# Kernel optimization log

Hardware: AMD Instinct MI355X
Metric: run time of the kernel (lower is better)

The kernel has to match this reference:

```python
import jax, jax.numpy as jnp
import numpy as np

S_LEN = 1024; HIDDEN = 2048; VOCAB = 32000; DFF = 6144
NK = 8; NV = 16; DK = 128; DV = 128; CONV_K = 4
CONV_DIM = 2 * NK * DK + NV * DV  # 4096
NQ = 16; NKV = 2; HD = 128; MAX_KV = 4096; SP = 512; CHUNK = 64


def silu(x):
    return x * jax.nn.sigmoid(x)


def rmsnorm(x, w, eps=1e-6):
    xf = x.astype(jnp.float32)
    return (xf * jax.lax.rsqrt(jnp.mean(xf * xf, -1, keepdims=True) + eps)) * w


def gated_rmsnorm(x, z, w, eps=1e-6):
    xf = x.astype(jnp.float32) * silu(z.astype(jnp.float32))
    return (xf * jax.lax.rsqrt(jnp.mean(xf * xf, -1, keepdims=True) + eps)) * w


def rotate_half(x):
    a, b = jnp.split(x, 2, -1)
    return jnp.concatenate([-b, a], -1)


def chunk_gated_delta_rule(q, k, v, g, beta, init_state, chunk=CHUNK):
    # q,k: [B,S,H,Dk]; v: [B,S,H,Dv]; g,beta: [B,S,H]; init_state: [B,H,Dk,Dv]
    q = q / jnp.sqrt(jnp.sum(q * q, -1, keepdims=True) + 1e-6)  # qk l2norm
    k = k / jnp.sqrt(jnp.sum(k * k, -1, keepdims=True) + 1e-6)
    tr = lambda x: x.transpose(0, 2, 1, 3).astype(jnp.float32)
    q, k, v = tr(q), tr(k), tr(v)
    g = g.transpose(0, 2, 1).astype(jnp.float32)
    beta = beta.transpose(0, 2, 1).astype(jnp.float32)
    B, H, S, Dk = q.shape
    Dv = v.shape[-1]
    N = S // chunk  # S is a multiple of chunk here (no padding needed)
    q = q * Dk ** -0.5
    rc = lambda x: x.reshape(B, H, N, chunk, x.shape[-1])
    q, k, v = rc(q), rc(k), rc(v)
    g = jnp.cumsum(g.reshape(B, H, N, chunk), -1)  # cumulative log-decay within chunk
    beta = beta.reshape(B, H, N, chunk)
    kb = k * beta[..., None]
    vb = v * beta[..., None]
    ii = jnp.arange(chunk)
    lower = ii[:, None] >= ii[None, :]
    strict = ii[:, None] > ii[None, :]
    decay = jnp.where(lower, jnp.exp(g[..., :, None] - g[..., None, :]), 0.0)
    # strictly-lower A; T = (I - A)^{-1} (exact triangular solve == converged Neumann series)
    A = -jnp.where(strict, jnp.einsum('bhnik,bhnjk->bhnij', kb, k) * decay, 0.0)
    eye = jnp.eye(chunk, dtype=jnp.float32)
    T = jax.scipy.linalg.solve_triangular(eye - A, jnp.broadcast_to(eye, A.shape), lower=True)
    w = jnp.einsum('bhnij,bhnjd->bhnid', T, vb)
    kc = jnp.einsum('bhnij,bhnjd->bhnid', T, kb * jnp.exp(g)[..., None])
    mv = lambda x: jnp.moveaxis(x, 2, 0)

    def step(state, xs):
        qi, ki, wi, kci, gi, di = xs
        attn = jnp.where(lower, jnp.einsum('bhik,bhjk->bhij', qi, ki) * di, 0.0)
        v_new = wi - jnp.einsum('bhik,bhkd->bhid', kci, state)
        out = jnp.einsum('bhik,bhkd->bhid', qi * jnp.exp(gi)[..., None], state) \
            + jnp.einsum('bhij,bhjd->bhid', attn, v_new)
        gl = gi[..., -1]
        kd = ki * jnp.exp(gl[..., None] - gi)[..., None]
        state = state * jnp.exp(gl)[..., None, None] + jnp.einsum('bhik,bhid->bhkd', kd, v_new)
        return state, out

    final, outs = jax.lax.scan(step, init_state.astype(jnp.float32),
                               (mv(q), mv(k), mv(w), mv(kc), mv(g), mv(decay)))
    out = jnp.moveaxis(outs, 0, 2).reshape(B, H, S, Dv).transpose(0, 2, 1, 3)  # [B,S,H,Dv]
    return out, final


def mlp(x, gw, uw, dw):
    return (silu(x @ gw) * (x @ uw)) @ dw


def model_forward(input_ids, start_pos, rope_cos, rope_sin, attn_mask, conv_state, rec_state,
                  key_cache, value_cache, embed_w, dl_ln_w, dl_qkv_w, conv_w, conv_b, dl_z_w,
                  dl_b_w, dl_a_w, A_log, dt_bias, dn_norm_w, dl_out_w, dl_post_ln_w, dl_gate_w,
                  dl_up_w, dl_down_w, al_ln_w, q_w, q_norm_w, k_w, k_norm_w, v_w, o_w,
                  al_post_ln_w, al_gate_w, al_up_w, al_down_w, final_norm_w, lm_head_w):
    B, S = input_ids.shape
    hidden = embed_w[input_ids]
    # ---------------- DeltaNet (linear attention) layer ----------------
    res = hidden
    x = rmsnorm(hidden, dl_ln_w)
    mixed = (x @ dl_qkv_w).transpose(0, 2, 1)             # [B, CONV_DIM, S]
    padded = jnp.concatenate([conv_state, mixed], -1)      # [B, CONV_DIM, K+S]
    L = padded.shape[-1] - (CONV_K - 1)
    conv = conv_b[:, None] + sum(conv_w[:, kk][:, None] * padded[:, :, kk:kk + L]
                                 for kk in range(CONV_K))  # depthwise conv1d
    mixed = silu(conv[:, :, -S:]).transpose(0, 2, 1)
    new_conv = padded[:, :, -CONV_K:]
    kd = NK * DK
    qq = mixed[..., :kd].reshape(B, S, NK, DK)
    kk_ = mixed[..., kd:2 * kd].reshape(B, S, NK, DK)
    vv = mixed[..., 2 * kd:].reshape(B, S, NV, DV)
    z = (x @ dl_z_w).reshape(B, S, NV, DV)
    beta = jax.nn.sigmoid(x @ dl_b_w)
    a = (x @ dl_a_w).astype(jnp.float32)
    g = -jnp.exp(A_log.astype(jnp.float32)) * jax.nn.softplus(a + dt_bias)
    rep = NV // NK
    qq = jnp.repeat(qq, rep, axis=2)
    kk_ = jnp.repeat(kk_, rep, axis=2)
    core, new_rec = chunk_gated_delta_rule(qq, kk_, vv, g, beta, rec_state)
    core = gated_rmsnorm(core.reshape(-1, DV), z.reshape(-1, DV), dn_norm_w).reshape(B, S, NV * DV)
    hidden = res + core @ dl_out_w
    hidden = hidden + mlp(rmsnorm(hidden, dl_post_ln_w), dl_gate_w, dl_up_w, dl_down_w)
    # ---------------- Full attention layer (gated GQA, KV-cache scatter) ----------------
    res = hidden
    x = rmsnorm(hidden, al_ln_w)
    qg = (x @ q_w).reshape(B, S, NQ, 2 * HD)
    query, gate = jnp.split(qg, 2, -1)
    gate = gate.reshape(B, S, NQ * HD)
    query = rmsnorm(query, q_norm_w).transpose(0, 2, 1, 3)               # [B,NQ,S,HD]
    key_new = rmsnorm((x @ k_w).reshape(B, S, NKV, HD), k_norm_w).transpose(0, 2, 1, 3)
    value_new = (x @ v_w).reshape(B, S, NKV, HD).transpose(0, 2, 1, 3)
    c = rope_cos[:, None]
    sn = rope_sin[:, None]
    query = query * c + rotate_half(query) * sn
    key_new = key_new * c + rotate_half(key_new) * sn
    new_kc = jax.lax.dynamic_update_slice(key_cache, key_new, (0, 0, start_pos, 0))
    new_vc = jax.lax.dynamic_update_slice(value_cache, value_new, (0, 0, start_pos, 0))
    ng = NQ // NKV
    k_rep = jnp.repeat(new_kc, ng, axis=1)
    v_rep = jnp.repeat(new_vc, ng, axis=1)
    scores = jnp.einsum('bhsd,bhtd->bhst', query, k_rep) * HD ** -0.5 + attn_mask
    probs = jax.nn.softmax(scores.astype(jnp.float32), -1).astype(query.dtype)
    ao = jnp.einsum('bhst,bhtd->bhsd', probs, v_rep).transpose(0, 2, 1, 3).reshape(B, S, NQ * HD)
    ao = ao * jax.nn.sigmoid(gate)
    hidden = res + ao @ o_w
    hidden = hidden + mlp(rmsnorm(hidden, al_post_ln_w), al_gate_w, al_up_w, al_down_w)
    logits = rmsnorm(hidden, final_norm_w) @ lm_head_w
    return logits, new_conv, new_rec, new_kc, new_vc


def setup_inputs():
    key = jax.random.key(0)
    ks = iter(jax.random.split(key, 64))
    def rn(shape, s=0.02):
        return jax.random.normal(next(ks), shape, jnp.float32) * s
    input_ids = jax.random.randint(next(ks), (1, S_LEN), 0, VOCAB)
    inv = 1.0 / (10000.0 ** (jnp.arange(0, HD, 2, dtype=jnp.float32) / HD))
    pos = jnp.arange(SP, SP + S_LEN, dtype=jnp.float32)
    fr = pos[:, None] * inv[None, :]
    emb = jnp.concatenate([fr, fr], -1)
    rope_cos = jnp.cos(emb)[None]
    rope_sin = jnp.sin(emb)[None]
    qpos = SP + jnp.arange(S_LEN)
    kpos = jnp.arange(MAX_KV)
    attn_mask = jnp.where(kpos[None, :] <= qpos[:, None], 0.0, -1e9).astype(jnp.float32)[None, None]
    return dict(
        input_ids=input_ids, seq_len=S_LEN, start_pos=SP,
        rope_cos=rope_cos, rope_sin=rope_sin, attn_mask=attn_mask,
        conv_state=rn((1, CONV_DIM, CONV_K), 1.0), rec_state=rn((1, NV, DK, DV), 1.0),
        key_cache=rn((1, NKV, MAX_KV, HD), 1.0), value_cache=rn((1, NKV, MAX_KV, HD), 1.0),
        embed_w=rn((VOCAB, HIDDEN)), dl_ln_w=jnp.ones(HIDDEN),
        dl_qkv_w=rn((HIDDEN, CONV_DIM)), conv_w=rn((CONV_DIM, CONV_K), 0.3),
        conv_b=rn((CONV_DIM,)), dl_z_w=rn((HIDDEN, NV * DV)),
        dl_b_w=rn((HIDDEN, NV)), dl_a_w=rn((HIDDEN, NV)),
        A_log=jnp.log(jnp.linspace(1.0, 8.0, NV)), dt_bias=rn((NV,), 0.1),
        dn_norm_w=jnp.ones(DV), dl_out_w=rn((NV * DV, HIDDEN)),
        dl_post_ln_w=jnp.ones(HIDDEN), dl_gate_w=rn((HIDDEN, DFF)),
        dl_up_w=rn((HIDDEN, DFF)), dl_down_w=rn((DFF, HIDDEN)),
        al_ln_w=jnp.ones(HIDDEN), q_w=rn((HIDDEN, NQ * HD * 2)), q_norm_w=jnp.ones(HD),
        k_w=rn((HIDDEN, NKV * HD)), k_norm_w=jnp.ones(HD), v_w=rn((HIDDEN, NKV * HD)),
        o_w=rn((NQ * HD, HIDDEN)), al_post_ln_w=jnp.ones(HIDDEN),
        al_gate_w=rn((HIDDEN, DFF)), al_up_w=rn((HIDDEN, DFF)), al_down_w=rn((DFF, HIDDEN)),
        final_norm_w=jnp.ones(HIDDEN), lm_head_w=rn((HIDDEN, VOCAB)))


def reference(input_ids, seq_len, start_pos, rope_cos, rope_sin, attn_mask, conv_state,
              rec_state, key_cache, value_cache, embed_w, dl_ln_w, dl_qkv_w, conv_w, conv_b,
              dl_z_w, dl_b_w, dl_a_w, A_log, dt_bias, dn_norm_w, dl_out_w, dl_post_ln_w,
              dl_gate_w, dl_up_w, dl_down_w, al_ln_w, q_w, q_norm_w, k_w, k_norm_w, v_w, o_w,
              al_post_ln_w, al_gate_w, al_up_w, al_down_w, final_norm_w, lm_head_w):
    del seq_len  # unused in original forward body (padding bookkeeping only)
    return model_forward(input_ids, start_pos, rope_cos, rope_sin, attn_mask, conv_state,
                         rec_state, key_cache, value_cache, embed_w, dl_ln_w, dl_qkv_w, conv_w,
                         conv_b, dl_z_w, dl_b_w, dl_a_w, A_log, dt_bias, dn_norm_w, dl_out_w,
                         dl_post_ln_w, dl_gate_w, dl_up_w, dl_down_w, al_ln_w, q_w, q_norm_w,
                         k_w, k_norm_w, v_w, o_w, al_post_ln_w, al_gate_w, al_up_w, al_down_w,
                         final_norm_w, lm_head_w)
```

## Files before the change

### kernel.cpp

```cpp
#include <hip/hip_runtime.h>
#include <math.h>

#define S_LEN 1024
#define HIDN  2048
#define NVH   16
#define CDIM  4096
#define MAXKV 4096
#define SP    512

typedef __attribute__((ext_vector_type(4))) float f32x4v;
typedef _Float16 f16x8 __attribute__((ext_vector_type(8)));
typedef unsigned short ushort_t;

__device__ __forceinline__ unsigned int pack2h(float a, float b) {
  auto h = __builtin_amdgcn_cvt_pkrtz(a, b);
  return __builtin_bit_cast(unsigned int, h);
}
__device__ __forceinline__ ushort_t h16(float x) {
  auto v = __builtin_amdgcn_cvt_pkrtz(x, x);
  return (ushort_t)__builtin_bit_cast(unsigned int, v);
}
__device__ __forceinline__ void gload16(const void* g, void* l) {
  __builtin_amdgcn_global_load_lds(
      (const __attribute__((address_space(1))) void*)(g),
      (__attribute__((address_space(3))) void*)(l), 16, 0, 0);
}

template<int TM, bool ACC>
__global__ __launch_bounds__(256) void gemm_h(const ushort_t* __restrict__ A16,
    const float* __restrict__ B, float* __restrict__ C, int M, int N, int K) {
  constexpr int MI = TM / 32;
  __shared__ ushort_t Al[TM * 32];
  __shared__ unsigned int Bl[4][128][4];
  const int tid = threadIdx.x;
  const int gm = M / TM;
  const int nwg = gridDim.x;
  const int q = nwg >> 3, r = nwg & 7;
  const int xcd = blockIdx.x & 7, ii = blockIdx.x >> 3;
  const int lin = (xcd < r) ? (xcd * (q + 1) + ii)
                            : (r * (q + 1) + (xcd - r) * q + ii);
  const int m0 = (lin % gm) * TM;
  const int n0 = (lin / gm) * 128;
  const int wave = tid >> 6, lane = tid & 63;
  const int wm = (wave >> 1) * (TM / 2), wn = (wave & 1) * 64;
  const int lr = lane & 15, lg = lane >> 4;
  const int bn = tid & 127, bkb = (tid >> 7) * 2;
  const size_t panstride = (size_t)(K >> 5) * 2048;
  const ushort_t* Apan = A16 + (size_t)(m0 >> 6) * panstride;
  const float* Bp = B + (size_t)(bkb * 8) * N + n0 + bn;
  float br[16];
  f32x4v acc[MI][4];
  #pragma unroll
  for (int i = 0; i < MI; ++i)
    #pragma unroll
    for (int j = 0; j < 4; ++j)
      #pragma unroll
      for (int r2 = 0; r2 < 4; ++r2) acc[i][j][r2] = 0.f;
  const int NT = K >> 5;
  #pragma unroll
  for (int j = 0; j < 16; ++j) br[j] = Bp[(size_t)j * N];
  for (int t = 0; t < NT; ++t) {
    __syncthreads();
    if (TM == 128) {
      #pragma unroll
      for (int i2 = 0; i2 < 2; ++i2) {
        int c = wave * 2 + i2;
        int kb = c >> 1, half = c & 1;
        gload16(Apan + half * panstride + (size_t)t * 2048 + kb * 512 + lane * 8,
                Al + kb * 1024 + half * 512);
      }
    } else {
      int kb = wave;
      gload16(Apan + (size_t)t * 2048 + kb * 512 + lane * 8, Al + kb * 512);
    }
    *(uint4*)&Bl[bkb][bn][0] = make_uint4(
        pack2h(br[0], br[1]), pack2h(br[2], br[3]),
        pack2h(br[4], br[5]), pack2h(br[6], br[7]));
    *(uint4*)&Bl[bkb + 1][bn][0] = make_uint4(
        pack2h(br[8], br[9]), pack2h(br[10], br[11]),
        pack2h(br[12], br[13]), pack2h(br[14], br[15]));
    if (t + 1 < NT) {
      Bp += (size_t)32 * N;
      #pragma unroll
      for (int j = 0; j < 16; ++j) br[j] = Bp[(size_t)j * N];
    }
    __syncthreads();
    f16x8 af[MI], bfr[4];
    #pragma unroll
    for (int mi = 0; mi < MI; ++mi)
      af[mi] = *(const f16x8*)&Al[lg * (TM * 8) + (wm + mi * 16 + lr) * 8];
    #pragma unroll
    for (int ni = 0; ni < 4; ++ni)
      bfr[ni] = *(const f16x8*)&Bl[lg][wn + ni * 16 + lr][0];
    #pragma unroll
    for (int mi = 0; mi < MI; ++mi)
      #pragma unroll
      for (int ni = 0; ni < 4; ++ni)
        acc[mi][ni] = __builtin_amdgcn_mfma_f32_16x16x32_f16(
            af[mi], bfr[ni], acc[mi][ni], 0, 0, 0);
  }
  #pragma unroll
  for (int mi = 0; mi < MI; ++mi) {
    #pragma unroll
    for (int ni = 0; ni < 4; ++ni) {
      const int rr = m0 + wm + mi * 16 + lg * 4;
      const int cc = n0 + wn + ni * 16 + lr;
      #pragma unroll
      for (int r2 = 0; r2 < 4; ++r2) {
        float* cp = C + (size_t)(rr + r2) * N + cc;
        if (ACC) *cp += acc[mi][ni][r2];
        else     *cp = acc[mi][ni][r2];
      }
    }
  }
}

template<int TM, bool ACC, bool FS>
__global__ __launch_bounds__(256) void gemm_f16(const float* __restrict__ A,
    const float* A2, const float* __restrict__ B,
    float* __restrict__ C, int M, int N, int K) {
  constexpr int MI = TM / 32;
  constexpr int AF = TM / 8;
  __shared__ unsigned int Al[4][TM][4];
  __shared__ unsigned int Bl[4][128][4];
  const int tid = threadIdx.x;
  const int gm = M / TM;
  const int nwg = gridDim.x;
  const int q = nwg >> 3, r = nwg & 7;
  const int xcd = blockIdx.x & 7, ii = blockIdx.x >> 3;
  const int lin = (xcd < r) ? (xcd * (q + 1) + ii)
                            : (r * (q + 1) + (xcd - r) * q + ii);
  const int m0 = (lin % gm) * TM;
  const int n0 = (lin / gm) * 128;
  const int wave = tid >> 6, lane = tid & 63;
  const int wm = (wave >> 1) * (TM / 2), wn = (wave & 1) * 64;
  const int lr = lane & 15, lg = lane >> 4;
  const int am  = (TM == 128) ? (tid >> 1) : (tid >> 2);
  const int akb = (TM == 128) ? ((tid & 1) * 2) : (tid & 3);
  const int bn = tid & 127, bkb = (tid >> 7) * 2;
  const float* Ap  = A + (size_t)(m0 + am) * K + akb * 8;
  const float* A2p = A2 + (size_t)(m0 + am) * K + akb * 8;
  const float* Bp = B + (size_t)(bkb * 8) * N + n0 + bn;
  float ar[AF], ar2[FS ? AF : 1], br[16];
  f32x4v acc[MI][4];
  #pragma unroll
  for (int i = 0; i < MI; ++i)
    #pragma unroll
    for (int j = 0; j < 4; ++j)
      #pragma unroll
      for (int r2 = 0; r2 < 4; ++r2) acc[i][j][r2] = 0.f;
  const int NT = K >> 5;
  #pragma unroll
  for (int q2 = 0; q2 < AF / 4; ++q2)
    *(float4*)&ar[q2 * 4] = *(const float4*)(Ap + q2 * 4);
  if (FS) {
    #pragma unroll
    for (int q2 = 0; q2 < AF / 4; ++q2)
      *(float4*)&ar2[q2 * 4] = *(const float4*)(A2p + q2 * 4);
  }
  #pragma unroll
  for (int j = 0; j < 16; ++j) br[j] = Bp[(size_t)j * N];
  for (int t = 0; t < NT; ++t) {
    __syncthreads();
    float av[AF];
    #pragma unroll
    for (int u = 0; u < AF; ++u) {
      float g = ar[u];
      av[u] = FS ? (g / (1.f + expf(-g))) * ar2[u] : g;
    }
    *(uint4*)&Al[akb][am][0] = make_uint4(
        pack2h(av[0], av[1]), pack2h(av[2], av[3]),
        pack2h(av[4], av[5]), pack2h(av[6], av[7]));
    if (TM == 128) {
      *(uint4*)&Al[akb + 1][am][0] = make_uint4(
          pack2h(av[8], av[9]), pack2h(av[10], av[11]),
          pack2h(av[12], av[13]), pack2h(av[14], av[15]));
    }
    *(uint4*)&Bl[bkb][bn][0] = make_uint4(
        pack2h(br[0], br[1]), pack2h(br[2], br[3]),
        pack2h(br[4], br[5]), pack2h(br[6], br[7]));
    *(uint4*)&Bl[bkb + 1][bn][0] = make_uint4(
        pack2h(br[8], br[9]), pack2h(br[10], br[11]),
        pack2h(br[12], br[13]), pack2h(br[14], br[15]));
    if (t + 1 < NT) {
      Ap += 32; A2p += 32; Bp += (size_t)32 * N;
      #pragma unroll
      for (int q2 = 0; q2 < AF / 4; ++q2)
        *(float4*)&ar[q2 * 4] = *(const float4*)(Ap + q2 * 4);
      if (FS) {
        #pragma unroll
        for (int q2 = 0; q2 < AF / 4; ++q2)
          *(float4*)&ar2[q2 * 4] = *(const float4*)(A2p + q2 * 4);
      }
      #pragma unroll
      for (int j = 0; j < 16; ++j) br[j] = Bp[(size_t)j * N];
    }
    __syncthreads();
    f16x8 af[MI], bfr[4];
    #pragma unroll
    for (int mi = 0; mi < MI; ++mi)
      af[mi] = *(const f16x8*)&Al[lg][wm + mi * 16 + lr][0];
    #pragma unroll
    for (int ni = 0; ni < 4; ++ni)
      bfr[ni] = *(const f16x8*)&Bl[lg][wn + ni * 16 + lr][0];
    #pragma unroll
    for (int mi = 0; mi < MI; ++mi)
      #pragma unroll
      for (int ni = 0; ni < 4; ++ni)
        acc[mi][ni] = __builtin_amdgcn_mfma_f32_16x16x32_f16(
            af[mi], bfr[ni], acc[mi][ni], 0, 0, 0);
  }
  #pragma unroll
  for (int mi = 0; mi < MI; ++mi) {
    #pragma unroll
    for (int ni = 0; ni < 4; ++ni) {
      const int rr = m0 + wm + mi * 16 + lg * 4;
      const int cc = n0 + wn + ni * 16 + lr;
      #pragma unroll
      for (int r2 = 0; r2 < 4; ++r2) {
        float* cp = C + (size_t)(rr + r2) * N + cc;
        if (ACC) *cp += acc[mi][ni][r2];
        else     *cp = acc[mi][ni][r2];
      }
    }
  }
}

__global__ __launch_bounds__(256) void embed_k(const int* __restrict__ ids,
    const float* __restrict__ emb, float* __restrict__ hid) {
  int t = blockIdx.x * 256 + threadIdx.x;
  int s = t >> 9;
  int c4 = (t & 511) * 4;
  *(float4*)(hid + (size_t)s * HIDN + c4) =
      *(const float4*)(emb + (size_t)ids[s] * HIDN + c4);
}

__global__ __launch_bounds__(256) void rmsnorm_k(const float* __restrict__ in,
    const float* __restrict__ w, float* __restrict__ out,
    ushort_t* __restrict__ x16) {
  const int row = blockIdx.x;
  const float* ip = in + (size_t)row * HIDN;
  float ss = 0.f;
  for (int c = threadIdx.x * 4; c < HIDN; c += 1024) {
    float4 v = *(const float4*)(ip + c);
    ss += v.x * v.x + v.y * v.y + v.z * v.z + v.w * v.w;
  }
  #pragma unroll
  for (int o = 32; o > 0; o >>= 1) ss += __shfl_down(ss, o, 64);
  __shared__ float sred[4];
  if ((threadIdx.x & 63) == 0) sred[threadIdx.x >> 6] = ss;
  __syncthreads();
  float tot = sred[0] + sred[1] + sred[2] + sred[3];
  float sc = 1.f / sqrtf(tot * (1.f / HIDN) + 1e-6f);
  const int m = row & 63, mp = row >> 6;
  ushort_t* xb = x16 + (size_t)mp * (HIDN >> 5) * 2048 + m * 8;
  for (int c = threadIdx.x * 4; c < HIDN; c += 1024) {
    float4 v = *(const float4*)(ip + c);
    float4 o = make_float4(v.x * sc * w[c], v.y * sc * w[c + 1],
                           v.z * sc * w[c + 2], v.w * sc * w[c + 3]);
    *(float4*)(out + (size_t)row * HIDN + c) = o;
    int kt = c >> 5, kb = (c >> 3) & 3, j = c & 7;
    *(uint2*)(xb + (size_t)kt * 2048 + kb * 512 + j) =
        make_uint2(pack2h(o.x, o.y), pack2h(o.z, o.w));
  }
}

__global__ __launch_bounds__(256) void newconv_k(const float* __restrict__ mixed,
                                                 float* __restrict__ nc) {
  int t = blockIdx.x * 256 + threadIdx.x;
  int c = t >> 2, kk = t & 3;
  nc[t] = mixed[(size_t)(1020 + kk) * CDIM + c];
}

__global__ __launch_bounds__(256) void conv_k(const float* __restrict__ mixed,
    const float* __restrict__ cstate, const float* __restrict__ cw,
    const float* __restrict__ cb, float* __restrict__ convo) {
  int idx = blockIdx.x * 256 + threadIdx.x;
  int c = idx & (CDIM - 1);
  int s = idx >> 12;
  float acc = cb[c];
  #pragma unroll
  for (int kk = 0; kk < 4; ++kk) {
    int j = s + 1 + kk;
    float pv = (j < 4) ? cstate[c * 4 + j] : mixed[(size_t)(j - 4) * CDIM + c];
    acc = fmaf(cw[c * 4 + kk], pv, acc);
  }
  convo[(size_t)s * CDIM + c] = acc / (1.f + expf(-acc));
}

__global__ __launch_bounds__(128) void qknorm_k(const float* __restrict__ convo,
    float* __restrict__ qn, float* __restrict__ kn) {
  const int b = blockIdx.x;
  const int h8 = b & 7, s = b >> 3;
  const int d = threadIdx.x;
  float qv = convo[(size_t)s * CDIM + h8 * 128 + d];
  float kv = convo[(size_t)s * CDIM + 1024 + h8 * 128 + d];
  __shared__ float sred[4];
  float pq = qv * qv, pk = kv * kv;
  #pragma unroll
  for (int o = 32; o > 0; o >>= 1) { pq += __shfl_down(pq, o, 64); pk += __shfl_down(pk, o, 64); }
  if ((d & 63) == 0) { sred[d >> 6] = pq; sred[2 + (d >> 6)] = pk; }
  __syncthreads();
  float sq = sred[0] + sred[1], sk = sred[2] + sred[3];
  qn[((size_t)h8 * S_LEN + s) * 128 + d] = qv * (1.f / sqrtf(sq + 1e-6f)) * 0.08838834764831845f;
  kn[((size_t)h8 * S_LEN + s) * 128 + d] = kv * (1.f / sqrtf(sk + 1e-6f));
}

__global__ __launch_bounds__(256) void betag_k(const float* __restrict__ x,
    const float* __restrict__ bw, const float* __restrict__ aw,
    const float* __restrict__ A_log, const float* __restrict__ dt_bias,
    float* __restrict__ beta, float* __restrict__ g) {
  __shared__ float sx[2048];
  __shared__ float rb[16][17], ra[16][17];
  const int s = blockIdx.x;
  for (int c = threadIdx.x; c < HIDN; c += 256) sx[c] = x[(size_t)s * HIDN + c];
  __syncthreads();
  const int h = threadIdx.x & 15, part = threadIdx.x >> 4;
  float accb = 0.f, acca = 0.f;
  for (int j = 0; j < 128; ++j) {
    int k = part * 128 + j;
    float xv = sx[k];
    accb = fmaf(xv, bw[(size_t)k * 16 + h], accb);
    acca = fmaf(xv, aw[(size_t)k * 16 + h], acca);
  }
  rb[part][h] = accb; ra[part][h] = acca;
  __syncthreads();
  if (threadIdx.x < 16) {
    const int hh = threadIdx.x;
    float sb = 0.f, sa = 0.f;
    for (int p = 0; p < 16; ++p) { sb += rb[p][hh]; sa += ra[p][hh]; }
    beta[(size_t)s * 16 + hh] = 1.f / (1.f + expf(-sb));
    float aa = sa + dt_bias[hh];
    float sp = (aa > 20.f) ? aa : log1pf(expf(aa));
    g[(size_t)s * 16 + hh] = -expf(A_log[hh]) * sp;
  }
}

__global__ __launch_bounds__(256) void delta_phase1(
    const float* __restrict__ qn, const float* __restrict__ kn,
    const float* __restrict__ convo, const float* __restrict__ beta,
    const float* __restrict__ g,
    float* __restrict__ Wb, ushort_t* __restrict__ KC16,
    ushort_t* __restrict__ Q16, ushort_t* __restrict__ K16,
    ushort_t* __restrict__ ATT16, float* __restrict__ GCb) {
  __shared__ float sK[64][129];
  __shared__ float sV[64][129];
  __shared__ float sQ[64][129];
  __shared__ float sT[64][64];
  __shared__ float sgc[64], sbeta[64], seg[64], sEgl[64];
  const int blk = blockIdx.x;
  const int n = blk & 15, h = blk >> 4;
  const int hq = h >> 1;
  const int r0 = n * 64;
  const int tid = threadIdx.x;
  const size_t hn = (size_t)h * 16 + n;
  for (int t = tid; t < 2048; t += 256) {
    int i = t >> 5, c4 = (t & 31) * 4;
    float4 kv = *(const float4*)(kn + ((size_t)hq * S_LEN + r0 + i) * 128 + c4);
    float4 qv = *(const float4*)(qn + ((size_t)hq * S_LEN + r0 + i) * 128 + c4);
    float4 vv = *(const float4*)(convo + (size_t)(r0 + i) * CDIM + 2048 + h * 128 + c4);
    sK[i][c4+0]=kv.x; sK[i][c4+1]=kv.y; sK[i][c4+2]=kv.z; sK[i][c4+3]=kv.w;
    sQ[i][c4+0]=qv.x; sQ[i][c4+1]=qv.y; sQ[i][c4+2]=qv.z; sQ[i][c4+3]=qv.w;
    sV[i][c4+0]=vv.x; sV[i][c4+1]=vv.y; sV[i][c4+2]=vv.z; sV[i][c4+3]=vv.w;
  }
  if (tid < 64) sbeta[tid] = beta[(size_t)(r0 + tid) * NVH + h];
  __syncthreads();
  if (tid == 0) {
    float acc = 0.f;
    for (int i = 0; i < 64; ++i) { acc += g[(size_t)(r0 + i) * NVH + h]; sgc[i] = acc; }
  }
  __syncthreads();
  if (tid < 64) {
    seg[tid] = expf(sgc[tid]);
    sEgl[tid] = expf(sgc[63] - sgc[tid]);
  }
  {
    const int ty = tid >> 4, tx = tid & 15;
    float a[4][4] = {};
    #pragma unroll 4
    for (int k = 0; k < 128; ++k) {
      float kr[4], kc_[4];
      #pragma unroll
      for (int di = 0; di < 4; ++di) kr[di] = sK[ty * 4 + di][k];
      #pragma unroll
      for (int dj = 0; dj < 4; ++dj) kc_[dj] = sK[tx * 4 + dj][k];
      #pragma unroll
      for (int di = 0; di < 4; ++di)
        #pragma unroll
        for (int dj = 0; dj < 4; ++dj)
          a[di][dj] = fmaf(kr[di], kc_[dj], a[di][dj]);
    }
    #pragma unroll
    for (int di = 0; di < 4; ++di) {
      int i = ty * 4 + di;
      #pragma unroll
      for (int dj = 0; dj < 4; ++dj) {
        int j = tx * 4 + dj;
        float v;
        if (i > j) v = sbeta[i] * a[di][dj] * expf(sgc[i] - sgc[j]);
        else v = (i == j) ? 1.f : 0.f;
        sT[i][j] = v;
      }
    }
  }
  __syncthreads();
  if (tid < 64) {
    const int c = tid;
    for (int i = 1; i < 64; ++i) {
      if (c <= i) {
        float acc = (c == i) ? 1.f : 0.f;
        for (int j = c; j < i; ++j) acc -= sT[i][j] * sT[j][c];
        sT[i][c] = acc;
      }
    }
  }
  __syncthreads();
  for (int t = tid; t < 1024; t += 256) {
    int i = t >> 4, dg = (t & 15) * 8;
    float aw[8] = {}, ak[8] = {};
    for (int j = 0; j <= i; ++j) {
      float tv = sT[i][j] * sbeta[j];
      float te = tv * seg[j];
      #pragma unroll
      for (int u = 0; u < 8; ++u) {
        aw[u] = fmaf(tv, sV[j][dg + u], aw[u]);
        ak[u] = fmaf(te, sK[j][dg + u], ak[u]);
      }
    }
    float* wp = Wb + (hn * 64 + i) * 128 + dg;
    *(float4*)wp = make_float4(aw[0], aw[1], aw[2], aw[3]);
    *(float4*)(wp + 4) = make_float4(aw[4], aw[5], aw[6], aw[7]);
    uint4 kc = make_uint4(pack2h(-ak[0], -ak[1]), pack2h(-ak[2], -ak[3]),
                          pack2h(-ak[4], -ak[5]), pack2h(-ak[6], -ak[7]));
    *(uint4*)(KC16 + hn * 8192 + (dg >> 3) * 512 + i * 8) = kc;
  }
  for (int t = tid; t < 1024; t += 256) {
    int i = t >> 4, dg = (t & 15) * 8;
    float e = seg[i];
    uint4 qv = make_uint4(
        pack2h(sQ[i][dg] * e, sQ[i][dg + 1] * e),
        pack2h(sQ[i][dg + 2] * e, sQ[i][dg + 3] * e),
        pack2h(sQ[i][dg + 4] * e, sQ[i][dg + 5] * e),
        pack2h(sQ[i][dg + 6] * e, sQ[i][dg + 7] * e));
    *(uint4*)(Q16 + hn * 8192 + (dg >> 3) * 512 + i * 8) = qv;
  }
  for (int t = tid; t < 1024; t += 256) {
    int kv = t & 127, ib = t >> 7;
    int i0 = ib * 8;
    uint4 kk2 = make_uint4(
        pack2h(sK[i0 + 0][kv] * sEgl[i0 + 0], sK[i0 + 1][kv] * sEgl[i0 + 1]),
        pack2h(sK[i0 + 2][kv] * sEgl[i0 + 2], sK[i0 + 3][kv] * sEgl[i0 + 3]),
        pack2h(sK[i0 + 4][kv] * sEgl[i0 + 4], sK[i0 + 5][kv] * sEgl[i0 + 5]),
        pack2h(sK[i0 + 6][kv] * sEgl[i0 + 6], sK[i0 + 7][kv] * sEgl[i0 + 7]));
    *(uint4*)(K16 + hn * 8192 + ib * 1024 + kv * 8) = kk2;
  }
  __syncthreads();
  {
    const int ty = tid >> 4, tx = tid & 15;
    float a[4][4] = {};
    #pragma unroll 4
    for (int k = 0; k < 128; ++k) {
      float qr[4], kc_[4];
      #pragma unroll
      for (int di = 0; di < 4; ++di) qr[di] = sQ[ty * 4 + di][k];
      #pragma unroll
      for (int dj = 0; dj < 4; ++dj) kc_[dj] = sK[tx * 4 + dj][k];
      #pragma unroll
      for (int di = 0; di < 4; ++di)
        #pragma unroll
        for (int dj = 0; dj < 4; ++dj)
          a[di][dj] = fmaf(qr[di], kc_[dj], a[di][dj]);
    }
    #pragma unroll
    for (int di = 0; di < 4; ++di) {
      int i = ty * 4 + di;
      #pragma unroll
      for (int dj = 0; dj < 4; ++dj) {
        int j = tx * 4 + dj;
        float v = 0.f;
        if (i >= j) v = a[di][dj] * expf(sgc[i] - sgc[j]);
        sT[i][j] = v;
      }
    }
  }
  __syncthreads();
  for (int t = tid; t < 512; t += 256) {
    int i = t >> 3, jb = t & 7;
    const float* ap = &sT[i][jb * 8];
    uint4 av = make_uint4(pack2h(ap[0], ap[1]), pack2h(ap[2], ap[3]),
                          pack2h(ap[4], ap[5]), pack2h(ap[6], ap[7]));
    *(uint4*)(ATT16 + hn * 4096 + jb * 512 + i * 8) = av;
  }
  if (tid < 64) GCb[hn * 64 + tid] = sgc[tid];
}

__global__ __launch_bounds__(256) void delta_phase2(
    const ushort_t* __restrict__ KC16, const ushort_t* __restrict__ Q16,
    const ushort_t* __restrict__ K16, const ushort_t* __restrict__ ATT16,
    const float* __restrict__ Wb, const float* __restrict__ GCb,
    const float* __restrict__ rec_state,
    float* __restrict__ core, float* __restrict__ new_rec) {
  __shared__ uint4 bufKC[1024];
  __shared__ uint4 bufQ[1024];
  __shared__ uint4 bufK[1024];
  __shared__ uint4 bufA[512];
  __shared__ uint4 bufS[512];
  __shared__ uint4 bufV[256];
  ushort_t* sKC = (ushort_t*)bufKC;
  ushort_t* sQ6 = (ushort_t*)bufQ;
  ushort_t* sK6 = (ushort_t*)bufK;
  ushort_t* sAT = (ushort_t*)bufA;
  ushort_t* sS  = (ushort_t*)bufS;
  ushort_t* sVn = (ushort_t*)bufV;
  const int h = blockIdx.x >> 2, ds = blockIdx.x & 3;
  const int d0 = ds * 32;
  const int tid = threadIdx.x;
  const int w = tid >> 6;
  const int lane = tid & 63, lr = lane & 15, lg = lane >> 4;
  const int rowS0 = w * 32;
  f32x4v aS[2][2];
  #pragma unroll
  for (int tm = 0; tm < 2; ++tm)
    #pragma unroll
    for (int tn = 0; tn < 2; ++tn)
      #pragma unroll
      for (int r = 0; r < 4; ++r) {
        int row = rowS0 + tm * 16 + lg * 4 + r;
        int col = tn * 16 + lr;
        aS[tm][tn][r] = rec_state[((size_t)h * 128 + row) * 128 + d0 + col];
      }
  for (int n = 0; n < 16; ++n) {
    const size_t hn = (size_t)h * 16 + n;
    const uint4* pKC = (const uint4*)(KC16 + hn * 8192);
    const uint4* pQ  = (const uint4*)(Q16  + hn * 8192);
    const uint4* pK  = (const uint4*)(K16  + hn * 8192);
    const uint4* pA  = (const uint4*)(ATT16 + hn * 4096);
    uint4 stKC[4], stQ[4], stK[4], stA[2];
    #pragma unroll
    for (int u = 0; u < 4; ++u) {
      stKC[u] = pKC[tid + u * 256];
      stQ[u]  = pQ[tid + u * 256];
      stK[u]  = pK[tid + u * 256];
    }
    #pragma unroll
    for (int u = 0; u < 2; ++u) stA[u] = pA[tid + u * 256];
    const float egl = expf(GCb[hn * 64 + 63]);
    float wseed[2][4];
    #pragma unroll
    for (int tn = 0; tn < 2; ++tn)
      #pragma unroll
      for (int r = 0; r < 4; ++r)
        wseed[tn][r] = Wb[(hn * 64 + (w * 16 + lg * 4 + r)) * 128 + d0 + tn * 16 + lr];
    #pragma unroll
    for (int tm = 0; tm < 2; ++tm)
      #pragma unroll
      for (int tn = 0; tn < 2; ++tn)
        #pragma unroll
        for (int r = 0; r < 4; ++r) {
          int row = rowS0 + tm * 16 + lg * 4 + r;
          int col = tn * 16 + lr;
          sS[(row >> 3) * 256 + col * 8 + (row & 7)] = h16(aS[tm][tn][r]);
        }
    #pragma unroll
    for (int u = 0; u < 4; ++u) {
      bufKC[tid + u * 256] = stKC[u];
      bufQ[tid + u * 256]  = stQ[u];
      bufK[tid + u * 256]  = stK[u];
    }
    #pragma unroll
    for (int u = 0; u < 2; ++u) bufA[tid + u * 256] = stA[u];
    __syncthreads();
    f32x4v aV[2];
    #pragma unroll
    for (int tn = 0; tn < 2; ++tn)
      #pragma unroll
      for (int r = 0; r < 4; ++r) aV[tn][r] = wseed[tn][r];
    #pragma unroll
    for (int c = 0; c < 4; ++c) {
      f16x8 a = *(const f16x8*)&sKC[((c * 4 + lg) * 64 + w * 16 + lr) * 8];
      #pragma unroll
      for (int tn = 0; tn < 2; ++tn) {
        f16x8 b = *(const f16x8*)&sS[((c * 4 + lg) * 32 + tn * 16 + lr) * 8];
        aV[tn] = __builtin_amdgcn_mfma_f32_16x16x32_f16(a, b, aV[tn], 0, 0, 0);
      }
    }
    #pragma unroll
    for (int tn = 0; tn < 2; ++tn)
      #pragma unroll
      for (int r = 0; r < 4; ++r) {
        int row = w * 16 + lg * 4 + r;
        int col = tn * 16 + lr;
        sVn[(row >> 3) * 256 + col * 8 + (row & 7)] = h16(aV[tn][r]);
      }
    __syncthreads();
    f32x4v aO[2];
    #pragma unroll
    for (int tn = 0; tn < 2; ++tn)
      #pragma unroll
      for (int r = 0; r < 4; ++r) aO[tn][r] = 0.f;
    #pragma unroll
    for (int c = 0; c < 4; ++c) {
      f16x8 a = *(const f16x8*)&sQ6[((c * 4 + lg) * 64 + w * 16 + lr) * 8];
      #pragma unroll
      for (int tn = 0; tn < 2; ++tn) {
        f16x8 b = *(const f16x8*)&sS[((c * 4 + lg) * 32 + tn * 16 + lr) * 8];
        aO[tn] = __builtin_amdgcn_mfma_f32_16x16x32_f16(a, b, aO[tn], 0, 0, 0);
      }
    }
    #pragma unroll
    for (int c = 0; c < 2; ++c) {
      f16x8 a = *(const f16x8*)&sAT[((c * 4 + lg) * 64 + w * 16 + lr) * 8];
      #pragma unroll
      for (int tn = 0; tn < 2; ++tn) {
        f16x8 b = *(const f16x8*)&sVn[((c * 4 + lg) * 32 + tn * 16 + lr) * 8];
        aO[tn] = __builtin_amdgcn_mfma_f32_16x16x32_f16(a, b, aO[tn], 0, 0, 0);
      }
    }
    #pragma unroll
    for (int tn = 0; tn < 2; ++tn)
      #pragma unroll
      for (int r = 0; r < 4; ++r) {
        int row = w * 16 + lg * 4 + r;
        core[(size_t)(n * 64 + row) * HIDN + h * 128 + d0 + tn * 16 + lr] = aO[tn][r];
      }
    #pragma unroll
    for (int tm = 0; tm < 2; ++tm)
      #pragma unroll
      for (int tn = 0; tn < 2; ++tn)
        #pragma unroll
        for (int r = 0; r < 4; ++r) aS[tm][tn][r] *= egl;
    #pragma unroll
    for (int tm = 0; tm < 2; ++tm) {
      #pragma unroll
      for (int c = 0; c < 2; ++c) {
        f16x8 a = *(const f16x8*)&sK6[((c * 4 + lg) * 128 + rowS0 + tm * 16 + lr) * 8];
        #pragma unroll
        for (int tn = 0; tn < 2; ++tn) {
          f16x8 b = *(const f16x8*)&sVn[((c * 4 + lg) * 32 + tn * 16 + lr) * 8];
          aS[tm][tn] = __builtin_amdgcn_mfma_f32_16x16x32_f16(a, b, aS[tm][tn], 0, 0, 0);
        }
      }
    }
    __syncthreads();
  }
  #pragma unroll
  for (int tm = 0; tm < 2; ++tm)
    #pragma unroll
    for (int tn = 0; tn < 2; ++tn)
      #pragma unroll
      for (int r = 0; r < 4; ++r) {
        int row = rowS0 + tm * 16 + lg * 4 + r;
        int col = tn * 16 + lr;
        new_rec[((size_t)h * 128 + row) * 128 + d0 + col] = aS[tm][tn][r];
      }
}

__global__ __launch_bounds__(128) void gatedrms_k(const float* __restrict__ core,
    const float* __restrict__ z, const float* __restrict__ w,
    ushort_t* __restrict__ c16) {
  const int b = blockIdx.x;
  const int h = b & 15, s = b >> 4;
  const int d = threadIdx.x;
  size_t idx = (size_t)s * HIDN + h * 128 + d;
  float cv = core[idx], zv = z[idx];
  float xf = cv * (zv / (1.f + expf(-zv)));
  __shared__ float sred[2];
  float ps = xf * xf;
  #pragma unroll
  for (int o = 32; o > 0; o >>= 1) ps += __shfl_down(ps, o, 64);
  if ((d & 63) == 0) sred[d >> 6] = ps;
  __syncthreads();
  float ss = sred[0] + sred[1];
  float val = xf * (1.f / sqrtf(ss * (1.f / 128.f) + 1e-6f)) * w[d];
  float nb = __shfl_down(val, 1, 64);
  if (!(d & 1)) {
    int c = h * 128 + d;
    int kt = c >> 5, kb = (c >> 3) & 3, j = c & 7;
    int m = s & 63, mp = s >> 6;
    *(unsigned int*)(c16 + (size_t)mp * 131072 + kt * 2048 + kb * 512 + m * 8 + j)
        = pack2h(val, nb);
  }
}

__global__ __launch_bounds__(128) void qrope_k(const float* __restrict__ qg,
    const float* __restrict__ qnw, const float* __restrict__ cosb,
    const float* __restrict__ sinb, float* __restrict__ qhat,
    float* __restrict__ agate) {
  const int b = blockIdx.x;
  const int h = b & 15, s = b >> 4;
  const int d = threadIdx.x;
  float qv = qg[(size_t)s * 4096 + h * 256 + d];
  float gv = qg[(size_t)s * 4096 + h * 256 + 128 + d];
  __shared__ float sred[2];
  float ps = qv * qv;
  #pragma unroll
  for (int o = 32; o > 0; o >>= 1) ps += __shfl_down(ps, o, 64);
  if ((d & 63) == 0) sred[d >> 6] = ps;
  __syncthreads();
  float ss = sred[0] + sred[1];
  float qn_ = qv * (1.f / sqrtf(ss * (1.f / 128.f) + 1e-6f)) * qnw[d];
  __shared__ float tmp[128];
  tmp[d] = qn_;
  __syncthreads();
  float other = tmp[d ^ 64];
  float rh = (d < 64) ? -other : other;
  float c = cosb[(size_t)s * 128 + d];
  float sn = sinb[(size_t)s * 128 + d];
  qhat[((size_t)h * S_LEN + s) * 128 + d] = qn_ * c + rh * sn;
  agate[(size_t)s * HIDN + h * 128 + d] = gv;
}

__global__ __launch_bounds__(128) void kvrope_k(const float* __restrict__ kraw,
    const float* __restrict__ vraw, const float* __restrict__ knw,
    const float* __restrict__ cosb, const float* __restrict__ sinb,
    float* __restrict__ kcache, float* __restrict__ vcache) {
  const int b = blockIdx.x;
  const int h2 = b & 1, s = b >> 1;
  const int d = threadIdx.x;
  float kv = kraw[(size_t)s * 256 + h2 * 128 + d];
  __shared__ float sred[2];
  float ps = kv * kv;
  #pragma unroll
  for (int o = 32; o > 0; o >>= 1) ps += __shfl_down(ps, o, 64);
  if ((d & 63) == 0) sred[d >> 6] = ps;
  __syncthreads();
  float ss = sred[0] + sred[1];
  float kn_ = kv * (1.f / sqrtf(ss * (1.f / 128.f) + 1e-6f)) * knw[d];
  __shared__ float tmp[128];
  tmp[d] = kn_;
  __syncthreads();
  float other = tmp[d ^ 64];
  float rh = (d < 64) ? -other : other;
  size_t row = (size_t)h2 * MAXKV + SP + s;
  kcache[row * 128 + d] = kn_ * cosb[(size_t)s * 128 + d] + rh * sinb[(size_t)s * 128 + d];
  vcache[row * 128 + d] = vraw[(size_t)s * 256 + h2 * 128 + d];
}

__global__ __launch_bounds__(256) void kv16_k(const float* __restrict__ kc,
    const float* __restrict__ vc, ushort_t* __restrict__ KV16) {
  const int b = blockIdx.x;
  const int kt = b % 24, h2 = b / 24;
  const int tid = threadIdx.x;
  const float* Kb = kc + ((size_t)h2 * MAXKV + kt * 64) * 128;
  const float* Vb = vc + ((size_t)h2 * MAXKV + kt * 64) * 128;
  ushort_t* Ko = KV16 + ((size_t)h2 * 24 + kt) * 8192;
  ushort_t* Vo = KV16 + 393216 + ((size_t)h2 * 24 + kt) * 8192;
  #pragma unroll
  for (int it = 0; it < 4; ++it) {
    int tt = tid + it * 256;
    int row = tt >> 4, kb = tt & 15;
    float4 a = *(const float4*)(Kb + row * 128 + kb * 8);
    float4 c = *(const float4*)(Kb + row * 128 + kb * 8 + 4);
    *(uint4*)(Ko + ((size_t)kb * 64 + row) * 8) = make_uint4(
        pack2h(a.x, a.y), pack2h(a.z, a.w), pack2h(c.x, c.y), pack2h(c.z, c.w));
  }
  #pragma unroll
  for (int it = 0; it < 4; ++it) {
    int tt = tid + it * 256;
    int key = tt >> 4, dg = tt & 15;
    float4 a = *(const float4*)(Vb + key * 128 + dg * 8);
    float4 c = *(const float4*)(Vb + key * 128 + dg * 8 + 4);
    int base = (key >> 3) * 1024 + (key & 7);
    Vo[base + (dg * 8 + 0) * 8] = h16(a.x);
    Vo[base + (dg * 8 + 1) * 8] = h16(a.y);
    Vo[base + (dg * 8 + 2) * 8] = h16(a.z);
    Vo[base + (dg * 8 + 3) * 8] = h16(a.w);
    Vo[base + (dg * 8 + 4) * 8] = h16(c.x);
    Vo[base + (dg * 8 + 5) * 8] = h16(c.y);
    Vo[base + (dg * 8 + 6) * 8] = h16(c.z);
    Vo[base + (dg * 8 + 7) * 8] = h16(c.w);
  }
}

__global__ __launch_bounds__(256) void attn_k(const float* __restrict__ qhat,
    const ushort_t* __restrict__ KV16,
    const float* __restrict__ agate, ushort_t* __restrict__ AO16) {
  __shared__ unsigned int Ql[16][64][4];
  __shared__ unsigned int Kl[16][64][4];
  __shared__ unsigned int Vl[8][128][4];
  __shared__ unsigned int Pl[8][64][4];
  const int h = blockIdx.x >> 4, qb = blockIdx.x & 15;
  const int hkv = h >> 3;
  const int tid = threadIdx.x;
  const int wave = tid >> 6, lane = tid & 63;
  const int lr = lane & 15, lg = lane >> 4;
  const float SCALE = 0.08838834764831845f;
  const float* Qb = qhat + ((size_t)h * S_LEN + qb * 64) * 128;
  #pragma unroll
  for (int it = 0; it < 4; ++it) {
    int tt = tid + it * 256;
    int row = tt >> 4, kb = tt & 15;
    float4 a = *(const float4*)(Qb + row * 128 + kb * 8);
    float4 b = *(const float4*)(Qb + row * 128 + kb * 8 + 4);
    *(uint4*)&Ql[kb][row][0] = make_uint4(
        pack2h(a.x * SCALE, a.y * SCALE), pack2h(a.z * SCALE, a.w * SCALE),
        pack2h(b.x * SCALE, b.y * SCALE), pack2h(b.z * SCALE, b.w * SCALE));
  }
  float m_run[4], l_run[4];
  #pragma unroll
  for (int r = 0; r < 4; ++r) { m_run[r] = -3.0e38f; l_run[r] = 0.f; }
  f32x4v accO[8];
  #pragma unroll
  for (int nd = 0; nd < 8; ++nd)
    #pragma unroll
    for (int r = 0; r < 4; ++r) accO[nd][r] = 0.f;
  const int ntiles = 9 + qb;
  for (int kt = 0; kt < ntiles; ++kt) {
    __syncthreads();
    const ushort_t* Ks = KV16 + ((size_t)hkv * 24 + kt) * 8192;
    const ushort_t* Vs = KV16 + 393216 + ((size_t)hkv * 24 + kt) * 8192;
    #pragma unroll
    for (int i2 = 0; i2 < 4; ++i2) {
      int c = wave * 4 + i2;
      gload16(Ks + (size_t)c * 512 + lane * 8, (char*)Kl + c * 1024);
      gload16(Vs + (size_t)c * 512 + lane * 8, (char*)Vl + c * 1024);
    }
    __syncthreads();
    f32x4v accS[4];
    #pragma unroll
    for (int ni = 0; ni < 4; ++ni)
      #pragma unroll
      for (int r = 0; r < 4; ++r) accS[ni][r] = 0.f;
    #pragma unroll
    for (int c = 0; c < 4; ++c) {
      f16x8 aq = *(const f16x8*)&Ql[c * 4 + lg][wave * 16 + lr][0];
      #pragma unroll
      for (int ni = 0; ni < 4; ++ni) {
        f16x8 bk = *(const f16x8*)&Kl[c * 4 + lg][ni * 16 + lr][0];
        accS[ni] = __builtin_amdgcn_mfma_f32_16x16x32_f16(aq, bk, accS[ni], 0, 0, 0);
      }
    }
    const bool boundary = (kt == ntiles - 1);
    float alpha[4];
    #pragma unroll
    for (int r = 0; r < 4; ++r) {
      const int qrow = wave * 16 + lg * 4 + r;
      float tm = -3.0e38f;
      #pragma unroll
      for (int ni = 0; ni < 4; ++ni) {
        if (boundary && (ni * 16 + lr) > qrow) accS[ni][r] = -3.0e38f;
        tm = fmaxf(tm, accS[ni][r]);
      }
      tm = fmaxf(tm, __shfl_xor(tm, 1, 64));
      tm = fmaxf(tm, __shfl_xor(tm, 2, 64));
      tm = fmaxf(tm, __shfl_xor(tm, 4, 64));
      tm = fmaxf(tm, __shfl_xor(tm, 8, 64));
      float mnew = fmaxf(m_run[r], tm);
      alpha[r] = expf(m_run[r] - mnew);
      m_run[r] = mnew;
      float ls = 0.f;
      #pragma unroll
      for (int ni = 0; ni < 4; ++ni) {
        float p = expf(accS[ni][r] - mnew);
        accS[ni][r] = p;
        ls += p;
      }
      ls += __shfl_xor(ls, 1, 64);
      ls += __shfl_xor(ls, 2, 64);
      ls += __shfl_xor(ls, 4, 64);
      ls += __shfl_xor(ls, 8, 64);
      l_run[r] = l_run[r] * alpha[r] + ls;
    }
    {
      _Float16* pp = (_Float16*)Pl;
      #pragma unroll
      for (int ni = 0; ni < 4; ++ni) {
        int key = ni * 16 + lr;
        int base = (key >> 3) * 512 + (key & 7);
        #pragma unroll
        for (int r = 0; r < 4; ++r) {
          int q = wave * 16 + lg * 4 + r;
          pp[base + q * 8] = (_Float16)accS[ni][r];
        }
      }
    }
    #pragma unroll
    for (int nd = 0; nd < 8; ++nd)
      #pragma unroll
      for (int r = 0; r < 4; ++r) accO[nd][r] *= alpha[r];
    #pragma unroll
    for (int c2 = 0; c2 < 2; ++c2) {
      f16x8 ap = *(const f16x8*)&Pl[c2 * 4 + lg][wave * 16 + lr][0];
      #pragma unroll
      for (int nd = 0; nd < 8; ++nd) {
        f16x8 bv = *(const f16x8*)&Vl[c2 * 4 + lg][nd * 16 + lr][0];
        accO[nd] = __builtin_amdgcn_mfma_f32_16x16x32_f16(ap, bv, accO[nd], 0, 0, 0);
      }
    }
  }
  #pragma unroll
  for (int r = 0; r < 4; ++r) {
    const int row = qb * 64 + wave * 16 + lg * 4 + r;
    const int m = row & 63, mp = row >> 6;
    const float inv = 1.f / l_run[r];
    #pragma unroll
    for (int nd = 0; nd < 8; ++nd) {
      int d = nd * 16 + lr;
      float gv = agate[(size_t)row * HIDN + h * 128 + d];
      float val = accO[nd][r] * inv * (1.f / (1.f + expf(-gv)));
      float nb = __shfl_down(val, 1, 64);
      if (!(lr & 1)) {
        int c = h * 128 + d;
        int kt2 = c >> 5, kb2 = (c >> 3) & 3, j2 = c & 7;
        *(unsigned int*)(AO16 + (size_t)mp * 131072 + kt2 * 2048 + kb2 * 512 + m * 8 + j2)
            = pack2h(val, nb);
      }
    }
  }
}

static inline void gemmh128(const ushort_t* A16, const float* B, float* C,
                            int M, int N, int K, hipStream_t st) {
  dim3 g((N / 128) * (M / 128));
  hipLaunchKernelGGL((gemm_h<128, false>), g, dim3(256), 0, st, A16, B, C, M, N, K);
}
static inline void gemmh64(const ushort_t* A16, const float* B, float* C,
                           int M, int N, int K, hipStream_t st) {
  dim3 g((N / 128) * (M / 64));
  hipLaunchKernelGGL((gemm_h<64, false>), g, dim3(256), 0, st, A16, B, C, M, N, K);
}
static inline void gemmh64a(const ushort_t* A16, const float* B, float* C,
                            int M, int N, int K, hipStream_t st) {
  dim3 g((N / 128) * (M / 64));
  hipLaunchKernelGGL((gemm_h<64, true>), g, dim3(256), 0, st, A16, B, C, M, N, K);
}
static inline void gemm128(const float* A, const float* B, float* C,
                           int M, int N, int K, bool acc, hipStream_t st) {
  dim3 g((N / 128) * (M / 128));
  if (acc) hipLaunchKernelGGL((gemm_f16<128, true,  false>), g, dim3(256), 0, st, A, A, B, C, M, N, K);
  else     hipLaunchKernelGGL((gemm_f16<128, false, false>), g, dim3(256), 0, st, A, A, B, C, M, N, K);
}
static inline void gemm_dn(const float* G, const float* U, const float* B, float* C,
                           int M, int N, int K, hipStream_t st) {
  dim3 g((N / 128) * (M / 64));
  hipLaunchKernelGGL((gemm_f16<64, true, true>), g, dim3(256), 0, st, G, U, B, C, M, N, K);
}

extern "C" void kernel_launch(void* const* d_in, const int* in_sizes, int n_in,
                              void* d_out, int out_size, void* d_ws, size_t ws_size,
                              hipStream_t stream) {
  (void)in_sizes; (void)n_in; (void)out_size;
  const int*   ids         = (const int*)  d_in[0];
  const float* rope_cos    = (const float*)d_in[3];
  const float* rope_sin    = (const float*)d_in[4];
  const float* conv_state  = (const float*)d_in[6];
  const float* rec_state   = (const float*)d_in[7];
  const float* key_cache   = (const float*)d_in[8];
  const float* value_cache = (const float*)d_in[9];
  const float* embed_w     = (const float*)d_in[10];
  const float* dl_ln_w     = (const float*)d_in[11];
  const float* dl_qkv_w    = (const float*)d_in[12];
  const float* conv_w      = (const float*)d_in[13];
  const float* conv_b      = (const float*)d_in[14];
  const float* dl_z_w      = (const float*)d_in[15];
  const float* dl_b_w      = (const float*)d_in[16];
  const float* dl_a_w      = (const float*)d_in[17];
  const float* A_log       = (const float*)d_in[18];
  const float* dt_bias     = (const float*)d_in[19];
  const float* dn_norm_w   = (const float*)d_in[20];
  const float* dl_out_w    = (const float*)d_in[21];
  const float* dl_post_ln  = (const float*)d_in[22];
  const float* dl_gate_w   = (const float*)d_in[23];
  const float* dl_up_w     = (const float*)d_in[24];
  const float* dl_down_w   = (const float*)d_in[25];
  const float* al_ln_w     = (const float*)d_in[26];
  const float* q_w         = (const float*)d_in[27];
  const float* q_norm_w    = (const float*)d_in[28];
  const float* k_w         = (const float*)d_in[29];
  const float* k_norm_w    = (const float*)d_in[30];
  const float* v_w         = (const float*)d_in[31];
  const float* o_w         = (const float*)d_in[32];
  const float* al_post_ln  = (const float*)d_in[33];
  const float* al_gate_w   = (const float*)d_in[34];
  const float* al_up_w     = (const float*)d_in[35];
  const float* al_down_w   = (const float*)d_in[36];
  const float* final_norm  = (const float*)d_in[37];
  const float* lm_head_w   = (const float*)d_in[38];

  float* out = (float*)d_out;
  float* logits   = out;
  float* new_conv = out + 32768000;
  float* new_rec  = out + 32784384;
  float* new_kc   = out + 33046528;
  float* new_vc   = out + 34095104;

  float* A_mixed = logits;
  float* A_convo = logits + 4194304;
  float* A_z     = logits + 8388608;
  float* A_qn    = logits + 10485760;
  float* A_kn    = logits + 11534336;
  float* A_w     = logits + 12582912;
  float* A_kc    = logits + 14680064;
  float* A_att   = logits + 16777216;
  float* A_gc    = logits + 17825792;
  float* A_core  = logits + 17842176;
  float* A_big0  = logits + 19939328;
  float* A_big1  = logits + 26230784;
  float* A_qhat  = A_big1;
  float* A_gate  = A_big1 + 2097152;
  float* A_kraw  = A_mixed;
  float* A_vraw  = A_mixed + 262144;

  ushort_t* KC16  = (ushort_t*)A_kc;
  ushort_t* K16   = (ushort_t*)A_kc + 2097152;
  ushort_t* Q16   = (ushort_t*)A_att;
  ushort_t* ATT16 = (ushort_t*)A_big0;
  ushort_t* KV16  = (ushort_t*)(A_big0 + 4194304);
  ushort_t* CORE16 = (ushort_t*)A_kn;
  ushort_t* AO16   = (ushort_t*)(A_mixed + 524288);

  float* ws     = (float*)d_ws;
  float* W_hid  = ws;
  float* W_x    = ws + 2097152;
  float* W_beta = ws + 4194304;
  float* W_g    = ws + 4210688;

  const bool ws_ok = (ws_size >= (size_t)21102592 + 65536);
  ushort_t* X16 = ws_ok ? (ushort_t*)(ws + 4227072)
                        : (ushort_t*)A_qn;

  hipLaunchKernelGGL(embed_k, dim3(2048), dim3(256), 0, stream, ids, embed_w, W_hid);
  hipLaunchKernelGGL(rmsnorm_k, dim3(1024), dim3(256), 0, stream, W_hid, dl_ln_w, W_x, X16);
  gemmh128(X16, dl_qkv_w, A_mixed, 1024, 4096, 2048, stream);
  hipLaunchKernelGGL(newconv_k, dim3(64), dim3(256), 0, stream, A_mixed, new_conv);
  hipLaunchKernelGGL(conv_k, dim3(16384), dim3(256), 0, stream,
                     A_mixed, conv_state, conv_w, conv_b, A_convo);
  gemmh64(X16, dl_z_w, A_z, 1024, 2048, 2048, stream);
  hipLaunchKernelGGL(betag_k, dim3(1024), dim3(256), 0, stream,
                     W_x, dl_b_w, dl_a_w, A_log, dt_bias, W_beta, W_g);
  hipLaunchKernelGGL(qknorm_k, dim3(8192), dim3(128), 0, stream, A_convo, A_qn, A_kn);
  hipLaunchKernelGGL(delta_phase1, dim3(256), dim3(256), 0, stream,
                     A_qn, A_kn, A_convo, W_beta, W_g,
                     A_w, KC16, Q16, K16, ATT16, A_gc);
  hipLaunchKernelGGL(delta_phase2, dim3(64), dim3(256), 0, stream,
                     KC16, Q16, K16, ATT16, A_w, A_gc, rec_state, A_core, new_rec);
  hipLaunchKernelGGL(gatedrms_k, dim3(16384), dim3(128), 0, stream,
                     A_core, A_z, dn_norm_w, CORE16);
  gemmh64a(CORE16, dl_out_w, W_hid, 1024, 2048, 2048, stream);
  hipLaunchKernelGGL(rmsnorm_k, dim3(1024), dim3(256), 0, stream, W_hid, dl_post_ln, W_x, X16);
  gemmh64(X16, dl_gate_w, A_big0, 1024, 6144, 2048, stream);
  gemmh64(X16, dl_up_w,   A_big1, 1024, 6144, 2048, stream);
  gemm_dn(A_big0, A_big1, dl_down_w, W_hid, 1024, 2048, 6144, stream);
  hipLaunchKernelGGL(rmsnorm_k, dim3(1024), dim3(256), 0, stream, W_hid, al_ln_w, W_x, X16);
  gemmh128(X16, q_w, A_big0, 1024, 4096, 2048, stream);
  hipLaunchKernelGGL(qrope_k, dim3(16384), dim3(128), 0, stream,
                     A_big0, q_norm_w, rope_cos, rope_sin, A_qhat, A_gate);
  gemmh64(X16, k_w, A_kraw, 1024, 256, 2048, stream);
  gemmh64(X16, v_w, A_vraw, 1024, 256, 2048, stream);
  hipMemcpyAsync(new_kc, key_cache,   (size_t)2 * MAXKV * 128 * 4, hipMemcpyDeviceToDevice, stream);
  hipMemcpyAsync(new_vc, value_cache, (size_t)2 * MAXKV * 128 * 4, hipMemcpyDeviceToDevice, stream);
  hipLaunchKernelGGL(kvrope_k, dim3(2048), dim3(128), 0, stream,
                     A_kraw, A_vraw, k_norm_w, rope_cos, rope_sin, new_kc, new_vc);
  hipLaunchKernelGGL(kv16_k, dim3(48), dim3(256), 0, stream, new_kc, new_vc, KV16);
  hipLaunchKernelGGL(attn_k, dim3(256), dim3(256), 0, stream,
                     A_qhat, KV16, A_gate, AO16);
  gemmh64a(AO16, o_w, W_hid, 1024, 2048, 2048, stream);
  hipLaunchKernelGGL(rmsnorm_k, dim3(1024), dim3(256), 0, stream, W_hid, al_post_ln, W_x, X16);
  gemmh64(X16, al_gate_w, A_big0, 1024, 6144, 2048, stream);
  gemmh64(X16, al_up_w,   A_big1, 1024, 6144, 2048, stream);
  gemm_dn(A_big0, A_big1, al_down_w, W_hid, 1024, 2048, 6144, stream);
  hipLaunchKernelGGL(rmsnorm_k, dim3(1024), dim3(256), 0, stream, W_hid, final_norm, W_x, X16);
  if (ws_ok) gemmh128(X16, lm_head_w, logits, 1024, 32000, 2048, stream);
  else       gemm128(W_x, lm_head_w, logits, 1024, 32000, 2048, false, stream);
}
```

Baseline: 1.675 ms.

## Pre-convert LM head weights to fp16 tiled layout and use fp16×fp16 GEMM

Adds a kernel that converts the fp32 lm_head weight into an fp16, panel-tiled buffer in a static device array on every call. A new GEMM then streams A and B through direct global-to-LDS loads and runs 16x16x32 fp16 MFMAs. The aim is to cut the fp32 B traffic and the in-loop conversion cost of the largest GEMM. In exchange it adds a full 262MB read and 131MB write of the weight per call, a 131MB static buffer, and a hipGetSymbolAddress call on the host path.

After: 1.714 ms. 1.02x slower.

```diff
diff --git a/kernel.cpp b/kernel.cpp
--- a/kernel.cpp
+++ b/kernel.cpp
@@ -7,10 +7,13 @@
 #define CDIM  4096
 #define MAXKV 4096
 #define SP    512
+#define LMN   32000
 
 typedef __attribute__((ext_vector_type(4))) float f32x4v;
 typedef _Float16 f16x8 __attribute__((ext_vector_type(8)));
 typedef unsigned short ushort_t;
+
+__device__ ushort_t g_LM16[65536000ULL];
 
 __device__ __forceinline__ unsigned int pack2h(float a, float b) {
   auto h = __builtin_amdgcn_cvt_pkrtz(a, b);
@@ -24,6 +27,95 @@
   __builtin_amdgcn_global_load_lds(
       (const __attribute__((address_space(1))) void*)(g),
       (__attribute__((address_space(3))) void*)(l), 16, 0, 0);
+}
+
+__global__ __launch_bounds__(256) void convw_lm(const float* __restrict__ W) {
+  int t = blockIdx.x * 256 + threadIdx.x;
+  int n_glob = t % LMN;
+  int kb_glob = t / LMN;
+  int kt = kb_glob >> 2, kb = kb_glob & 3;
+  int np = n_glob >> 7, n = n_glob & 127;
+  const float* src = W + (size_t)(kt * 32 + kb * 8) * LMN + n_glob;
+  float v0 = src[0];
+  float v1 = src[(size_t)LMN];
+  float v2 = src[(size_t)2 * LMN];
+  float v3 = src[(size_t)3 * LMN];
+  float v4 = src[(size_t)4 * LMN];
+  float v5 = src[(size_t)5 * LMN];
+  float v6 = src[(size_t)6 * LMN];
+  float v7 = src[(size_t)7 * LMN];
+  *(uint4*)(g_LM16 + ((size_t)np * 64 + kt) * 4096 + (size_t)((kb << 7) + n) * 8)
+      = make_uint4(pack2h(v0, v1), pack2h(v2, v3), pack2h(v4, v5), pack2h(v6, v7));
+}
+
+__global__ __launch_bounds__(256) void gemm_hh(const ushort_t* __restrict__ A16,
+    const ushort_t* __restrict__ B16, float* __restrict__ C, int M, int N, int K) {
+  __shared__ ushort_t Al[4096];
+  __shared__ ushort_t Bl[4096];
+  const int tid = threadIdx.x;
+  const int gm = M >> 7;
+  const int nwg = gridDim.x;
+  const int q = nwg >> 3, r = nwg & 7;
+  const int xcd = blockIdx.x & 7, ii = blockIdx.x >> 3;
+  const int lin = (xcd < r) ? (xcd * (q + 1) + ii)
+                            : (r * (q + 1) + (xcd - r) * q + ii);
+  const int m0 = (lin % gm) * 128;
+  const int n0 = (lin / gm) * 128;
+  const int wave = tid >> 6, lane = tid & 63;
+  const int wm = (wave >> 1) * 64, wn = (wave & 1) * 64;
+  const int lr = lane & 15, lg = lane >> 4;
+  const int NT = K >> 5;
+  const size_t panA = (size_t)NT * 2048;
+  const ushort_t* ApanL = A16 + (size_t)(m0 >> 6) * panA;
+  const ushort_t* ApanH = ApanL + panA;
+  const ushort_t* Bpan = B16 + (size_t)(n0 >> 7) * NT * 4096;
+  f32x4v acc[4][4];
+  #pragma unroll
+  for (int i = 0; i < 4; ++i)
+    #pragma unroll
+    for (int j = 0; j < 4; ++j)
+      #pragma unroll
+      for (int r2 = 0; r2 < 4; ++r2) acc[i][j][r2] = 0.f;
+  for (int t = 0; t < NT; ++t) {
+    __syncthreads();
+    #pragma unroll
+    for (int i2 = 0; i2 < 2; ++i2) {
+      int c = wave * 2 + i2;
+      int kb = c >> 1, hf = c & 1;
+      gload16((hf ? ApanH : ApanL) + (size_t)t * 2048 + kb * 512 + lane * 8,
+              Al + kb * 1024 + hf * 512);
+    }
+    #pragma unroll
+    for (int i2 = 0; i2 < 2; ++i2) {
+      int c = wave * 2 + i2;
+      gload16(Bpan + (size_t)t * 4096 + c * 512 + lane * 8, Bl + c * 512);
+    }
+    __syncthreads();
+    f16x8 af[4], bfr[4];
+    #pragma unroll
+    for (int mi = 0; mi < 4; ++mi)
+      af[mi] = *(const f16x8*)&Al[lg * 1024 + (wm + mi * 16 + lr) * 8];
+    #pragma unroll
+    for (int ni = 0; ni < 4; ++ni)
+      bfr[ni] = *(const f16x8*)&Bl[lg * 1024 + (wn + ni * 16 + lr) * 8];
+    #pragma unroll
+    for (int mi = 0; mi < 4; ++mi)
+      #pragma unroll
+      for (int ni = 0; ni < 4; ++ni)
+        acc[mi][ni] = __builtin_amdgcn_mfma_f32_16x16x32_f16(
+            af[mi], bfr[ni], acc[mi][ni], 0, 0, 0);
+  }
+  #pragma unroll
+  for (int mi = 0; mi < 4; ++mi) {
+    #pragma unroll
+    for (int ni = 0; ni < 4; ++ni) {
+      const int rr = m0 + wm + mi * 16 + lg * 4;
+      const int cc = n0 + wn + ni * 16 + lr;
+      #pragma unroll
+      for (int r2 = 0; r2 < 4; ++r2)
+        C[(size_t)(rr + r2) * N + cc] = acc[mi][ni][r2];
+    }
+  }
 }
 
 template<int TM, bool ACC>
@@ -1060,6 +1152,13 @@
   gemmh64(X16, al_up_w,   A_big1, 1024, 6144, 2048, stream);
   gemm_dn(A_big0, A_big1, al_down_w, W_hid, 1024, 2048, 6144, stream);
   hipLaunchKernelGGL(rmsnorm_k, dim3(1024), dim3(256), 0, stream, W_hid, final_norm, W_x, X16);
-  if (ws_ok) gemmh128(X16, lm_head_w, logits, 1024, 32000, 2048, stream);
-  else       gemm128(W_x, lm_head_w, logits, 1024, 32000, 2048, false, stream);
-}
+  if (ws_ok) {
+    hipLaunchKernelGGL(convw_lm, dim3(32000), dim3(256), 0, stream, lm_head_w);
+    ushort_t* lm16 = nullptr;
+    hipGetSymbolAddress((void**)&lm16, HIP_SYMBOL(g_LM16));
+    dim3 g((LMN / 128) * (1024 / 128));
+    hipLaunchKernelGGL(gemm_hh, g, dim3(256), 0, stream, X16, lm16, logits, 1024, LMN, 2048);
+  } else {
+    gemm128(W_x, lm_head_w, logits, 1024, LMN, 2048, false, stream);
+  }
+}
```
